# Optimization experiments

Measured on AMD Instinct MI355X. Metric: run time of the kernel, lower is better.

Reference implementation:

```python
import jax, jax.numpy as jnp
import numpy as np

N_NODES = 50000
N_EDGES = 800000
D_IN, D_HID, D_OUT = 128, 64, 64


def gcn_conv(x, W, b, src, dst, num_nodes):
    """PyG-style GCNConv: add self-loops, symmetric norm, aggregate at target.
    src/dst already include self-loops. x: [N, Din], W: [Din, Dout]."""
    xw = x @ W  # transform first (Din -> Dout), like PyG
    ew = jnp.ones(src.shape[0], dtype=x.dtype)
    deg = jax.ops.segment_sum(ew, dst, num_segments=num_nodes)
    dis = jnp.where(deg > 0, jax.lax.rsqrt(deg), 0.0)  # deg^{-1/2}
    norm = dis[src] * ew * dis[dst]  # [E+N]
    msgs = norm[:, None] * xw[src]  # gather source features
    out = jax.ops.segment_sum(msgs, dst, num_segments=num_nodes)
    return out + b


def setup_inputs() -> dict:
    key = jax.random.key(0)
    ks = jax.random.split(key, 8)
    x = jax.random.normal(ks[0], (N_NODES, D_IN), dtype=jnp.float32)
    edge_index = jax.random.randint(ks[1], (2, N_EDGES), 0, N_NODES, dtype=jnp.int64)
    W1 = jax.random.normal(ks[2], (D_IN, D_HID), dtype=jnp.float32) * (1.0 / np.sqrt(D_IN))
    b1 = jnp.zeros((D_HID,), dtype=jnp.float32)
    W2 = jax.random.normal(ks[3], (D_HID, D_HID), dtype=jnp.float32) * (1.0 / np.sqrt(D_HID))
    b2 = jnp.zeros((D_HID,), dtype=jnp.float32)
    W3 = jax.random.normal(ks[4], (D_HID, D_OUT), dtype=jnp.float32) * (1.0 / np.sqrt(D_HID))
    b3 = jnp.zeros((D_OUT,), dtype=jnp.float32)
    return {"x": x, "edge_index": edge_index, "W1": W1, "b1": b1,
            "W2": W2, "b2": b2, "W3": W3, "b3": b3}


def reference(x, edge_index, W1, b1, W2, b2, W3, b3):
    # Add self-loops once (shared by all layers), as PyG GCNConv does per layer.
    loop = jnp.arange(N_NODES, dtype=edge_index.dtype)
    src = jnp.concatenate([edge_index[0], loop])
    dst = jnp.concatenate([edge_index[1], loop])
    # Layer 1 + ReLU (dropout is identity in eval mode)
    h = gcn_conv(x, W1, b1, src, dst, N_NODES)
    h = jax.nn.relu(h)
    # Layer 2 + ReLU
    h = gcn_conv(h, W2, b2, src, dst, N_NODES)
    h = jax.nn.relu(h)
    # Layer 3 (no activation)
    out = gcn_conv(h, W3, b3, src, dst, N_NODES)
    return out
```

## Files before the change

kernel.cpp:

```cpp
#include <hip/hip_runtime.h>
#include <hip/hip_fp16.h>

#define N_NODES 50000
#define N_PAD   50048
#define N_EDGES 800000
#define D_IN    128
#define D_HID   64

#define NB         196
#define EB_CHUNK   4096
#define BIN_BLOCKS 196
#define ESTRIDE    4864
#define CSTRIDE    (ESTRIDE + 256)

typedef __bf16 bf16x8 __attribute__((ext_vector_type(8)));
typedef float  f32x4  __attribute__((ext_vector_type(4)));


template <int K>
__device__ __forceinline__ void pack_w(const float* __restrict__ W,
                                       __bf16* __restrict__ Bh, __bf16* __restrict__ Bl, int i) {
  constexpr int KS = K / 32;
  int j = i & 7, lane = (i >> 3) & 63, rest = i >> 9;
  int ct = rest / KS, ks = rest - ct * KS;
  int k = ks * 32 + ((lane >> 4) << 3) + j;
  int c = ct * 16 + (lane & 15);
  float v = W[k * 64 + c];
  __bf16 hb = (__bf16)v;
  Bh[i] = hb;
  Bl[i] = (__bf16)(v - (float)hb);
}


__global__ __launch_bounds__(256) void k_bins_sw(const int* __restrict__ src,
                                                 const int* __restrict__ dst,
                                                 unsigned* __restrict__ bucket_fill,
                                                 unsigned* __restrict__ temp,
                                                 const float* __restrict__ W1,
                                                 const float* __restrict__ W2,
                                                 const float* __restrict__ W3,
                                                 __bf16* __restrict__ Wh1, __bf16* __restrict__ Wl1,
                                                 __bf16* __restrict__ Wh2, __bf16* __restrict__ Wl2,
                                                 __bf16* __restrict__ Wh3, __bf16* __restrict__ Wl3) {
  __shared__ unsigned lh[256], lcur[256];
  int blk = blockIdx.x, t = threadIdx.x;
  if (blk >= BIN_BLOCKS) {
    int b = blk - BIN_BLOCKS;
    if (b < 32)      pack_w<D_IN >(W1, Wh1, Wl1, b * 256 + t);
    else if (b < 48) pack_w<D_HID>(W2, Wh2, Wl2, (b - 32) * 256 + t);
    else             pack_w<D_HID>(W3, Wh3, Wl3, (b - 48) * 256 + t);
    return;
  }
  lh[t] = 0;
  __syncthreads();
  int base = blk * EB_CHUNK;
  int endv = min(base + EB_CHUNK, N_EDGES);
  for (int e = base + t; e < endv; e += 256)
    atomicAdd(&lh[((unsigned)dst[e]) >> 8], 1u);
  __syncthreads();
  unsigned c = lh[t];
  lcur[t] = t * ESTRIDE + (c ? atomicAdd(&bucket_fill[t], c) : 0u);
  __syncthreads();
  for (int e = base + t; e < endv; e += 256) {
    unsigned d = (unsigned)dst[e];
    unsigned pos = atomicAdd(&lcur[d >> 8], 1u);
    temp[pos] = (unsigned)src[e] | ((d & 255u) << 16);
  }
}


template <int K, bool FIRST>
__device__ __forceinline__ void gemm_body(int bid,
                                          const float* __restrict__ Xf,
                                          const __bf16* __restrict__ Bh,
                                          const __bf16* __restrict__ Bl,
                                          __half* __restrict__ Y) {
  constexpr int KS = K / 32;
  const int tid  = threadIdx.x;
  const int wave = tid >> 6;
  const int lane = tid & 63;
  const int row0 = bid * 64 + wave * 16;
  const int row_a = min(row0 + (lane & 15), N_NODES - 1);
  const int q8 = (lane >> 4) << 3;

  f32x4 acc[4];
#pragma unroll
  for (int ct = 0; ct < 4; ct++) acc[ct] = (f32x4){0.f, 0.f, 0.f, 0.f};

#pragma unroll
  for (int ks = 0; ks < KS; ks++) {
    bf16x8 ah, al;
    const float4* xr4 = reinterpret_cast<const float4*>(Xf + (size_t)row_a * K);
    float4 f0 = xr4[ks * 8 + (q8 >> 2) + 0];
    float4 f1 = xr4[ks * 8 + (q8 >> 2) + 1];
#pragma unroll
    for (int j = 0; j < 4; j++) {
      float a0 = (&f0.x)[j], a1 = (&f1.x)[j];
      __bf16 h0 = (__bf16)a0, h1 = (__bf16)a1;
      ah[j] = h0;     al[j] = (__bf16)(a0 - (float)h0);
      ah[4 + j] = h1; al[4 + j] = (__bf16)(a1 - (float)h1);
    }
#pragma unroll
    for (int ct = 0; ct < 4; ct++) {
      bf16x8 bh = *reinterpret_cast<const bf16x8*>(Bh + (size_t)((ct * KS + ks) * 64 + lane) * 8);
      bf16x8 bl = *reinterpret_cast<const bf16x8*>(Bl + (size_t)((ct * KS + ks) * 64 + lane) * 8);
      acc[ct] = __builtin_amdgcn_mfma_f32_16x16x32_bf16(ah, bh, acc[ct], 0, 0, 0);
      acc[ct] = __builtin_amdgcn_mfma_f32_16x16x32_bf16(ah, bl, acc[ct], 0, 0, 0);
      acc[ct] = __builtin_amdgcn_mfma_f32_16x16x32_bf16(al, bh, acc[ct], 0, 0, 0);
    }
  }

  const int rbase = row0 + ((lane >> 4) << 2);
  const int c     = lane & 15;
#pragma unroll
  for (int ct = 0; ct < 4; ct++)
#pragma unroll
    for (int r = 0; r < 4; r++) {
      int row = rbase + r;
      if (row < N_NODES)
        Y[(size_t)row * 64 + ct * 16 + c] = __float2half_rn(acc[ct][r]);
    }
}


__global__ __launch_bounds__(256) void k_csr_gemm1(const unsigned* __restrict__ temp,
                                                   const unsigned* __restrict__ bucket_fill,
                                                   unsigned* __restrict__ rowptr,
                                                   unsigned* __restrict__ rowend,
                                                   float* __restrict__ dis,
                                                   unsigned short* __restrict__ csr,
                                                   const float* __restrict__ x,
                                                   const __bf16* __restrict__ Wh1,
                                                   const __bf16* __restrict__ Wl1,
                                                   __half* __restrict__ xw) {
  __shared__ unsigned hist[256], sscan[256], lfill[256];
  if (blockIdx.x >= NB) {
    gemm_body<D_IN, true>(blockIdx.x - NB, x, Wh1, Wl1, xw);
    return;
  }
  int b = blockIdx.x, t = threadIdx.x;
  unsigned ebase = b * ESTRIDE, ecnt = bucket_fill[b], cbase = b * CSTRIDE;
  int nodes = min(256, N_NODES - b * 256);
  hist[t] = 0;
  __syncthreads();
  for (unsigned i = t; i < ecnt; i += 256)
    atomicAdd(&hist[(temp[ebase + i] >> 16) & 255u], 1u);
  __syncthreads();
  unsigned deg = (t < nodes) ? hist[t] + 1u : 0u;
  sscan[t] = deg;
  __syncthreads();
  for (int off = 1; off < 256; off <<= 1) {
    unsigned v = (t >= off) ? sscan[t - off] : 0u;
    __syncthreads();
    sscan[t] += v;
    __syncthreads();
  }
  unsigned excl = sscan[t] - deg;
  if (t < nodes) {
    int node = b * 256 + t;
    rowptr[node] = cbase + excl;
    rowend[node] = cbase + excl + deg;
    dis[node] = rsqrtf((float)deg);
    csr[cbase + excl] = (unsigned short)node;
  }
  lfill[t] = excl + 1u;
  __syncthreads();
  for (unsigned i = t; i < ecnt; i += 256) {
    unsigned v = temp[ebase + i];
    unsigned d = (v >> 16) & 255u;
    unsigned pos = atomicAdd(&lfill[d], 1u);
    csr[cbase + pos] = (unsigned short)(v & 0xFFFFu);
  }
}


__device__ __forceinline__ void agg_core(int node, int lane, int sub, int grp,
                                         const float4* __restrict__ XW4,
                                         const unsigned* __restrict__ rowptr,
                                         const unsigned* __restrict__ rowend,
                                         const unsigned short* __restrict__ csr,
                                         const float* __restrict__ dis,
                                         float* __restrict__ accout) {
  const float disd = dis[node];
  unsigned beg = rowptr[node], end = rowend[node];
  float acc0[8] = {0,0,0,0,0,0,0,0};
  float acc1[8] = {0,0,0,0,0,0,0,0};

  for (unsigned j = beg; j < end; j += 64) {
    int nj = (int)min(64u, end - j);
    unsigned s = 0u; float nrm = 0.f;
    if (lane < nj) {
      s = csr[j + lane];
      nrm = dis[s] * disd;
    }
    for (int k = 0; k < nj; k += 16) {
      int e0 = k + grp;
      unsigned s0 = (unsigned)__shfl((int)s, e0);
      float    n0 = __shfl(nrm, e0);
      float4 v0 = XW4[(size_t)s0 * 8 + sub];
      const __half2* h0 = reinterpret_cast<const __half2*>(&v0);
#pragma unroll
      for (int q = 0; q < 4; q++) {
        float2 f = __half22float2(h0[q]);
        acc0[2*q]   += n0 * f.x;
        acc0[2*q+1] += n0 * f.y;
      }
      if (k + 8 < nj) {
        int e1 = k + grp + 8;
        unsigned s1 = (unsigned)__shfl((int)s, e1);
        float    n1 = __shfl(nrm, e1);
        float4 v1 = XW4[(size_t)s1 * 8 + sub];
        const __half2* h1 = reinterpret_cast<const __half2*>(&v1);
#pragma unroll
        for (int q = 0; q < 4; q++) {
          float2 f = __half22float2(h1[q]);
          acc1[2*q]   += n1 * f.x;
          acc1[2*q+1] += n1 * f.y;
        }
      }
    }
  }

#pragma unroll
  for (int i = 0; i < 8; i++) {
    float a = acc0[i] + acc1[i];
    a += __shfl_xor(a, 8);
    a += __shfl_xor(a, 16);
    a += __shfl_xor(a, 32);
    accout[i] = a;
  }
}


__global__ __launch_bounds__(1024) void k_agg_gemm(const float4* __restrict__ XW4,
                                                   const unsigned* __restrict__ rowptr,
                                                   const unsigned* __restrict__ rowend,
                                                   const unsigned short* __restrict__ csr,
                                                   const float* __restrict__ dis,
                                                   const float4* __restrict__ bias4,
                                                   const __bf16* __restrict__ Bh,
                                                   const __bf16* __restrict__ Bl,
                                                   __half* __restrict__ Y) {
  __shared__ float hld[16][68];
  const int wave = threadIdx.x >> 6;
  const int lane = threadIdx.x & 63;
  const int sub  = lane & 7;
  const int grp  = lane >> 3;
  const int node = blockIdx.x * 16 + wave;

  float acc[8];
  agg_core(node, lane, sub, grp, XW4, rowptr, rowend, csr, dis, acc);

  if (grp == 0) {
    float4 ba = bias4[sub * 2], bb = bias4[sub * 2 + 1];
    acc[0] += ba.x; acc[1] += ba.y; acc[2] += ba.z; acc[3] += ba.w;
    acc[4] += bb.x; acc[5] += bb.y; acc[6] += bb.z; acc[7] += bb.w;
    float4 o0, o1;
    o0.x = fmaxf(acc[0], 0.f); o0.y = fmaxf(acc[1], 0.f);
    o0.z = fmaxf(acc[2], 0.f); o0.w = fmaxf(acc[3], 0.f);
    o1.x = fmaxf(acc[4], 0.f); o1.y = fmaxf(acc[5], 0.f);
    o1.z = fmaxf(acc[6], 0.f); o1.w = fmaxf(acc[7], 0.f);
    *reinterpret_cast<float4*>(&hld[wave][sub * 8])     = o0;
    *reinterpret_cast<float4*>(&hld[wave][sub * 8 + 4]) = o1;
  }
  __syncthreads();

  if (wave < 4) {
    const int ct = wave;
    const int r16 = lane & 15;
    const int q8  = (lane >> 4) << 3;
    f32x4 gacc = (f32x4){0.f, 0.f, 0.f, 0.f};
#pragma unroll
    for (int ks = 0; ks < 2; ks++) {
      float4 f0 = *reinterpret_cast<const float4*>(&hld[r16][ks * 32 + q8]);
      float4 f1 = *reinterpret_cast<const float4*>(&hld[r16][ks * 32 + q8 + 4]);
      bf16x8 ah, al;
#pragma unroll
      for (int j = 0; j < 4; j++) {
        float a0 = (&f0.x)[j], a1 = (&f1.x)[j];
        __bf16 h0 = (__bf16)a0, h1 = (__bf16)a1;
        ah[j] = h0;     al[j] = (__bf16)(a0 - (float)h0);
        ah[4 + j] = h1; al[4 + j] = (__bf16)(a1 - (float)h1);
      }
      bf16x8 bh = *reinterpret_cast<const bf16x8*>(Bh + (size_t)((ct * 2 + ks) * 64 + lane) * 8);
      bf16x8 bl = *reinterpret_cast<const bf16x8*>(Bl + (size_t)((ct * 2 + ks) * 64 + lane) * 8);
      gacc = __builtin_amdgcn_mfma_f32_16x16x32_bf16(ah, bh, gacc, 0, 0, 0);
      gacc = __builtin_amdgcn_mfma_f32_16x16x32_bf16(ah, bl, gacc, 0, 0, 0);
      gacc = __builtin_amdgcn_mfma_f32_16x16x32_bf16(al, bh, gacc, 0, 0, 0);
    }
    const int rbase = blockIdx.x * 16 + ((lane >> 4) << 2);
    const int c     = lane & 15;
#pragma unroll
    for (int r = 0; r < 4; r++)
      Y[(size_t)(rbase + r) * 64 + ct * 16 + c] = __float2half_rn(gacc[r]);
  }
}


__global__ __launch_bounds__(256) void k_agg3(const float4* __restrict__ XW4,
                                              const unsigned* __restrict__ rowptr,
                                              const unsigned* __restrict__ rowend,
                                              const unsigned short* __restrict__ csr,
                                              const float* __restrict__ dis,
                                              const float4* __restrict__ bias4,
                                              float4* __restrict__ OUT4) {
  int node = (int)((blockIdx.x * blockDim.x + threadIdx.x) >> 6);
  int lane = threadIdx.x & 63;
  if (node >= N_NODES) return;
  const int sub = lane & 7;
  const int grp = lane >> 3;

  float acc[8];
  agg_core(node, lane, sub, grp, XW4, rowptr, rowend, csr, dis, acc);

  if (grp == 0) {
    float4 ba = bias4[sub * 2], bb = bias4[sub * 2 + 1];
    float4 o0 = {acc[0] + ba.x, acc[1] + ba.y, acc[2] + ba.z, acc[3] + ba.w};
    float4 o1 = {acc[4] + bb.x, acc[5] + bb.y, acc[6] + bb.z, acc[7] + bb.w};
    OUT4[(size_t)node * 16 + sub * 2]     = o0;
    OUT4[(size_t)node * 16 + sub * 2 + 1] = o1;
  }
}


extern "C" void kernel_launch(void* const* d_in, const int* in_sizes, int n_in,
                              void* d_out, int out_size, void* d_ws, size_t ws_size,
                              hipStream_t stream) {
  const float* x    = (const float*)d_in[0];
  const int*   eidx = (const int*)d_in[1];
  const float* W1   = (const float*)d_in[2];
  const float* b1   = (const float*)d_in[3];
  const float* W2   = (const float*)d_in[4];
  const float* b2   = (const float*)d_in[5];
  const float* W3   = (const float*)d_in[6];
  const float* b3   = (const float*)d_in[7];
  float* out = (float*)d_out;

  const int* e_src = eidx;
  const int* e_dst = eidx + N_EDGES;

  size_t off = 0;
  auto alloc = [&](size_t bytes) -> void* {
    void* p = (char*)d_ws + off;
    off += (bytes + 255) & ~(size_t)255;
    return p;
  };
  unsigned*       rowptr = (unsigned*)alloc((size_t)N_NODES * 4);
  unsigned*       rowend = (unsigned*)alloc((size_t)N_NODES * 4);
  float*          dis    = (float*)alloc((size_t)N_NODES * 4);
  unsigned short* csr    = (unsigned short*)alloc((size_t)NB * CSTRIDE * 2);
  unsigned*       temp   = (unsigned*)alloc((size_t)NB * ESTRIDE * 4);
  unsigned*       bfill  = (unsigned*)alloc(256 * 4);
  __half*         xwA    = (__half*)alloc((size_t)N_PAD * 64 * 2);
  __half*         xwB    = (__half*)alloc((size_t)N_PAD * 64 * 2);
  __bf16*         Wh1    = (__bf16*)alloc((size_t)D_IN * 64 * 2);
  __bf16*         Wl1    = (__bf16*)alloc((size_t)D_IN * 64 * 2);
  __bf16*         Wh2    = (__bf16*)alloc((size_t)D_HID * 64 * 2);
  __bf16*         Wl2    = (__bf16*)alloc((size_t)D_HID * 64 * 2);
  __bf16*         Wh3    = (__bf16*)alloc((size_t)D_HID * 64 * 2);
  __bf16*         Wl3    = (__bf16*)alloc((size_t)D_HID * 64 * 2);

  const int gemm_grid  = N_PAD / 64;
  const int fused_grid = N_NODES / 16;
  const int agg_grid   = (N_NODES * 64 + 255) / 256;

  hipMemsetAsync(bfill, 0, 256 * 4, stream);
  k_bins_sw<<<BIN_BLOCKS + 64, 256, 0, stream>>>(e_src, e_dst, bfill, temp,
                                                 W1, W2, W3, Wh1, Wl1, Wh2, Wl2, Wh3, Wl3);
  k_csr_gemm1<<<NB + gemm_grid, 256, 0, stream>>>(temp, bfill, rowptr, rowend,
                                                  dis, csr, x, Wh1, Wl1, xwA);
  k_agg_gemm<<<fused_grid, 1024, 0, stream>>>((const float4*)xwA, rowptr, rowend, csr, dis,
                                              (const float4*)b1, Wh2, Wl2, xwB);
  k_agg_gemm<<<fused_grid, 1024, 0, stream>>>((const float4*)xwB, rowptr, rowend, csr, dis,
                                              (const float4*)b2, Wh3, Wl3, xwA);
  k_agg3<<<agg_grid, 256, 0, stream>>>((const float4*)xwA, rowptr, rowend, csr, dis,
                                       (const float4*)b3, (float4*)out);
}
```

Measured before the change: 125.3 us.

## Fuse all GCN stages into one cooperative persistent kernel with grid syncs

```diff
diff --git a/kernel.cpp b/kernel.cpp
--- a/kernel.cpp
+++ b/kernel.cpp
@@ -1,5 +1,8 @@
 #include <hip/hip_runtime.h>
 #include <hip/hip_fp16.h>
+#include <hip/hip_cooperative_groups.h>
+
+namespace cg = cooperative_groups;
 
 #define N_NODES 50000
 #define N_PAD   50048
@@ -9,12 +12,22 @@
 
 #define NB         196
 #define EB_CHUNK   4096
-#define BIN_BLOCKS 196
 #define ESTRIDE    4864
 #define CSTRIDE    (ESTRIDE + 256)
 
 typedef __bf16 bf16x8 __attribute__((ext_vector_type(8)));
 typedef float  f32x4  __attribute__((ext_vector_type(4)));
+
+struct MegaParams {
+  const int* e_src; const int* e_dst;
+  unsigned* bfill; unsigned* temp;
+  const float* W1; const float* W2; const float* W3;
+  __bf16 *Wh1, *Wl1, *Wh2, *Wl2, *Wh3, *Wl3;
+  unsigned* rowptr; unsigned* rowend; float* dis; unsigned short* csr;
+  const float* x; __half* xwA; __half* xwB;
+  const float4 *b1, *b2, *b3;
+  float4* out;
+};
 
 
 template <int K>
@@ -32,51 +45,12 @@
 }
 
 
-__global__ __launch_bounds__(256) void k_bins_sw(const int* __restrict__ src,
-                                                 const int* __restrict__ dst,
-                                                 unsigned* __restrict__ bucket_fill,
-                                                 unsigned* __restrict__ temp,
-                                                 const float* __restrict__ W1,
-                                                 const float* __restrict__ W2,
-                                                 const float* __restrict__ W3,
-                                                 __bf16* __restrict__ Wh1, __bf16* __restrict__ Wl1,
-                                                 __bf16* __restrict__ Wh2, __bf16* __restrict__ Wl2,
-                                                 __bf16* __restrict__ Wh3, __bf16* __restrict__ Wl3) {
-  __shared__ unsigned lh[256], lcur[256];
-  int blk = blockIdx.x, t = threadIdx.x;
-  if (blk >= BIN_BLOCKS) {
-    int b = blk - BIN_BLOCKS;
-    if (b < 32)      pack_w<D_IN >(W1, Wh1, Wl1, b * 256 + t);
-    else if (b < 48) pack_w<D_HID>(W2, Wh2, Wl2, (b - 32) * 256 + t);
-    else             pack_w<D_HID>(W3, Wh3, Wl3, (b - 48) * 256 + t);
-    return;
-  }
-  lh[t] = 0;
-  __syncthreads();
-  int base = blk * EB_CHUNK;
-  int endv = min(base + EB_CHUNK, N_EDGES);
-  for (int e = base + t; e < endv; e += 256)
-    atomicAdd(&lh[((unsigned)dst[e]) >> 8], 1u);
-  __syncthreads();
-  unsigned c = lh[t];
-  lcur[t] = t * ESTRIDE + (c ? atomicAdd(&bucket_fill[t], c) : 0u);
-  __syncthreads();
-  for (int e = base + t; e < endv; e += 256) {
-    unsigned d = (unsigned)dst[e];
-    unsigned pos = atomicAdd(&lcur[d >> 8], 1u);
-    temp[pos] = (unsigned)src[e] | ((d & 255u) << 16);
-  }
-}
-
-
-template <int K, bool FIRST>
-__device__ __forceinline__ void gemm_body(int bid,
+__device__ __forceinline__ void gemm1_sub(int bid, int tid,
                                           const float* __restrict__ Xf,
                                           const __bf16* __restrict__ Bh,
                                           const __bf16* __restrict__ Bl,
                                           __half* __restrict__ Y) {
-  constexpr int KS = K / 32;
-  const int tid  = threadIdx.x;
+  constexpr int K = D_IN, KS = K / 32;
   const int wave = tid >> 6;
   const int lane = tid & 63;
   const int row0 = bid * 64 + wave * 16;
@@ -120,57 +94,6 @@
       if (row < N_NODES)
         Y[(size_t)row * 64 + ct * 16 + c] = __float2half_rn(acc[ct][r]);
     }
-}
-
-
-__global__ __launch_bounds__(256) void k_csr_gemm1(const unsigned* __restrict__ temp,
-                                                   const unsigned* __restrict__ bucket_fill,
-                                                   unsigned* __restrict__ rowptr,
-                                                   unsigned* __restrict__ rowend,
-                                                   float* __restrict__ dis,
-                                                   unsigned short* __restrict__ csr,
-                                                   const float* __restrict__ x,
-                                                   const __bf16* __restrict__ Wh1,
-                                                   const __bf16* __restrict__ Wl1,
-                                                   __half* __restrict__ xw) {
-  __shared__ unsigned hist[256], sscan[256], lfill[256];
-  if (blockIdx.x >= NB) {
-    gemm_body<D_IN, true>(blockIdx.x - NB, x, Wh1, Wl1, xw);
-    return;
-  }
-  int b = blockIdx.x, t = threadIdx.x;
-  unsigned ebase = b * ESTRIDE, ecnt = bucket_fill[b], cbase = b * CSTRIDE;
-  int nodes = min(256, N_NODES - b * 256);
-  hist[t] = 0;
-  __syncthreads();
-  for (unsigned i = t; i < ecnt; i += 256)
-    atomicAdd(&hist[(temp[ebase + i] >> 16) & 255u], 1u);
-  __syncthreads();
-  unsigned deg = (t < nodes) ? hist[t] + 1u : 0u;
-  sscan[t] = deg;
-  __syncthreads();
-  for (int off = 1; off < 256; off <<= 1) {
-    unsigned v = (t >= off) ? sscan[t - off] : 0u;
-    __syncthreads();
-    sscan[t] += v;
-    __syncthreads();
-  }
-  unsigned excl = sscan[t] - deg;
-  if (t < nodes) {
-    int node = b * 256 + t;
-    rowptr[node] = cbase + excl;
-    rowend[node] = cbase + excl + deg;
-    dis[node] = rsqrtf((float)deg);
-    csr[cbase + excl] = (unsigned short)node;
-  }
-  lfill[t] = excl + 1u;
-  __syncthreads();
-  for (unsigned i = t; i < ecnt; i += 256) {
-    unsigned v = temp[ebase + i];
-    unsigned d = (v >> 16) & 255u;
-    unsigned pos = atomicAdd(&lfill[d], 1u);
-    csr[cbase + pos] = (unsigned short)(v & 0xFFFFu);
-  }
 }
 
 
@@ -232,21 +155,21 @@
 }
 
 
-__global__ __launch_bounds__(1024) void k_agg_gemm(const float4* __restrict__ XW4,
-                                                   const unsigned* __restrict__ rowptr,
-                                                   const unsigned* __restrict__ rowend,
-                                                   const unsigned short* __restrict__ csr,
-                                                   const float* __restrict__ dis,
-                                                   const float4* __restrict__ bias4,
-                                                   const __bf16* __restrict__ Bh,
-                                                   const __bf16* __restrict__ Bl,
-                                                   __half* __restrict__ Y) {
-  __shared__ float hld[16][68];
-  const int wave = threadIdx.x >> 6;
-  const int lane = threadIdx.x & 63;
+__device__ __forceinline__ void agg_gemm_tile(int v, int t, float (*hld)[68],
+                                              const float4* __restrict__ XW4,
+                                              const unsigned* __restrict__ rowptr,
+                                              const unsigned* __restrict__ rowend,
+                                              const unsigned short* __restrict__ csr,
+                                              const float* __restrict__ dis,
+                                              const float4* __restrict__ bias4,
+                                              const __bf16* __restrict__ Bh,
+                                              const __bf16* __restrict__ Bl,
+                                              __half* __restrict__ Y) {
+  const int wave = t >> 6;
+  const int lane = t & 63;
   const int sub  = lane & 7;
   const int grp  = lane >> 3;
-  const int node = blockIdx.x * 16 + wave;
+  const int node = v * 16 + wave;
 
   float acc[8];
   agg_core(node, lane, sub, grp, XW4, rowptr, rowend, csr, dis, acc);
@@ -288,37 +211,120 @@
       gacc = __builtin_amdgcn_mfma_f32_16x16x32_bf16(ah, bl, gacc, 0, 0, 0);
       gacc = __builtin_amdgcn_mfma_f32_16x16x32_bf16(al, bh, gacc, 0, 0, 0);
     }
-    const int rbase = blockIdx.x * 16 + ((lane >> 4) << 2);
+    const int rbase = v * 16 + ((lane >> 4) << 2);
     const int c     = lane & 15;
 #pragma unroll
     for (int r = 0; r < 4; r++)
       Y[(size_t)(rbase + r) * 64 + ct * 16 + c] = __float2half_rn(gacc[r]);
   }
-}
-
-
-__global__ __launch_bounds__(256) void k_agg3(const float4* __restrict__ XW4,
-                                              const unsigned* __restrict__ rowptr,
-                                              const unsigned* __restrict__ rowend,
-                                              const unsigned short* __restrict__ csr,
-                                              const float* __restrict__ dis,
-                                              const float4* __restrict__ bias4,
-                                              float4* __restrict__ OUT4) {
-  int node = (int)((blockIdx.x * blockDim.x + threadIdx.x) >> 6);
-  int lane = threadIdx.x & 63;
-  if (node >= N_NODES) return;
-  const int sub = lane & 7;
-  const int grp = lane >> 3;
-
-  float acc[8];
-  agg_core(node, lane, sub, grp, XW4, rowptr, rowend, csr, dis, acc);
-
-  if (grp == 0) {
-    float4 ba = bias4[sub * 2], bb = bias4[sub * 2 + 1];
-    float4 o0 = {acc[0] + ba.x, acc[1] + ba.y, acc[2] + ba.z, acc[3] + ba.w};
-    float4 o1 = {acc[4] + bb.x, acc[5] + bb.y, acc[6] + bb.z, acc[7] + bb.w};
-    OUT4[(size_t)node * 16 + sub * 2]     = o0;
-    OUT4[(size_t)node * 16 + sub * 2 + 1] = o1;
+  __syncthreads();
+}
+
+
+__global__ __launch_bounds__(1024) void k_mega(MegaParams p) {
+  cg::grid_group grid = cg::this_grid();
+  __shared__ unsigned smem[4 * 768];
+  __shared__ float hld[16][68];
+  const int bid = blockIdx.x;
+  const int t   = threadIdx.x;
+  const int sb  = t >> 8, st = t & 255;
+
+  if (bid == 0 && t < 256) p.bfill[t] = 0;
+  grid.sync();
+
+  if (bid < 49) {
+    int v = bid * 4 + sb;
+    unsigned* lh   = smem + sb * 512;
+    unsigned* lcur = lh + 256;
+    lh[st] = 0;
+    __syncthreads();
+    int base = v * EB_CHUNK;
+    int endv = min(base + EB_CHUNK, N_EDGES);
+    for (int e = base + st; e < endv; e += 256)
+      atomicAdd(&lh[((unsigned)p.e_dst[e]) >> 8], 1u);
+    __syncthreads();
+    unsigned c = lh[st];
+    lcur[st] = st * ESTRIDE + (c ? atomicAdd(&p.bfill[st], c) : 0u);
+    __syncthreads();
+    for (int e = base + st; e < endv; e += 256) {
+      unsigned d = (unsigned)p.e_dst[e];
+      unsigned pos = atomicAdd(&lcur[d >> 8], 1u);
+      p.temp[pos] = (unsigned)p.e_src[e] | ((d & 255u) << 16);
+    }
+  } else if (bid < 65) {
+    int b = (bid - 49) * 4 + sb;
+    if (b < 32)      pack_w<D_IN >(p.W1, p.Wh1, p.Wl1, b * 256 + st);
+    else if (b < 48) pack_w<D_HID>(p.W2, p.Wh2, p.Wl2, (b - 32) * 256 + st);
+    else             pack_w<D_HID>(p.W3, p.Wh3, p.Wl3, (b - 48) * 256 + st);
+  }
+  grid.sync();
+
+  if (bid < 49) {
+    int b = bid * 4 + sb;
+    unsigned* hist  = smem + sb * 768;
+    unsigned* sscan = hist + 256;
+    unsigned* lfill = sscan + 256;
+    unsigned ebase = b * ESTRIDE, ecnt = p.bfill[b], cbase = b * CSTRIDE;
+    int nodes = min(256, N_NODES - b * 256);
+    hist[st] = 0;
+    __syncthreads();
+    for (unsigned i = st; i < ecnt; i += 256)
+      atomicAdd(&hist[(p.temp[ebase + i] >> 16) & 255u], 1u);
+    __syncthreads();
+    unsigned deg = (st < nodes) ? hist[st] + 1u : 0u;
+    sscan[st] = deg;
+    __syncthreads();
+    for (int off = 1; off < 256; off <<= 1) {
+      unsigned v2 = (st >= off) ? sscan[st - off] : 0u;
+      __syncthreads();
+      sscan[st] += v2;
+      __syncthreads();
+    }
+    unsigned excl = sscan[st] - deg;
+    if (st < nodes) {
+      int node = b * 256 + st;
+      p.rowptr[node] = cbase + excl;
+      p.rowend[node] = cbase + excl + deg;
+      p.dis[node] = rsqrtf((float)deg);
+      p.csr[cbase + excl] = (unsigned short)node;
+    }
+    lfill[st] = excl + 1u;
+    __syncthreads();
+    for (unsigned i = st; i < ecnt; i += 256) {
+      unsigned v2 = p.temp[ebase + i];
+      unsigned d = (v2 >> 16) & 255u;
+      unsigned pos = atomicAdd(&lfill[d], 1u);
+      p.csr[cbase + pos] = (unsigned short)(v2 & 0xFFFFu);
+    }
+  } else {
+    int v = (bid - 49) * 4 + sb;
+    if (v < 782) gemm1_sub(v, st, p.x, p.Wh1, p.Wl1, p.xwA);
+  }
+  grid.sync();
+
+  for (int v = bid; v < 3125; v += 256)
+    agg_gemm_tile(v, t, hld, (const float4*)p.xwA, p.rowptr, p.rowend, p.csr, p.dis,
+                  p.b1, p.Wh2, p.Wl2, p.xwB);
+  grid.sync();
+
+  for (int v = bid; v < 3125; v += 256)
+    agg_gemm_tile(v, t, hld, (const float4*)p.xwB, p.rowptr, p.rowend, p.csr, p.dis,
+                  p.b2, p.Wh3, p.Wl3, p.xwA);
+  grid.sync();
+
+  for (int v = bid; v < 3125; v += 256) {
+    const int wave = t >> 6, lane = t & 63;
+    const int sub = lane & 7, grp = lane >> 3;
+    const int node = v * 16 + wave;
+    float acc[8];
+    agg_core(node, lane, sub, grp, (const float4*)p.xwA, p.rowptr, p.rowend, p.csr, p.dis, acc);
+    if (grp == 0) {
+      float4 ba = p.b3[sub * 2], bb = p.b3[sub * 2 + 1];
+      float4 o0 = {acc[0] + ba.x, acc[1] + ba.y, acc[2] + ba.z, acc[3] + ba.w};
+      float4 o1 = {acc[4] + bb.x, acc[5] + bb.y, acc[6] + bb.z, acc[7] + bb.w};
+      p.out[(size_t)node * 16 + sub * 2]     = o0;
+      p.out[(size_t)node * 16 + sub * 2 + 1] = o1;
+    }
   }
 }
 
@@ -334,10 +340,6 @@
   const float* b2   = (const float*)d_in[5];
   const float* W3   = (const float*)d_in[6];
   const float* b3   = (const float*)d_in[7];
-  float* out = (float*)d_out;
-
-  const int* e_src = eidx;
-  const int* e_dst = eidx + N_EDGES;
 
   size_t off = 0;
   auto alloc = [&](size_t bytes) -> void* {
@@ -360,19 +362,16 @@
   __bf16*         Wh3    = (__bf16*)alloc((size_t)D_HID * 64 * 2);
   __bf16*         Wl3    = (__bf16*)alloc((size_t)D_HID * 64 * 2);
 
-  const int gemm_grid  = N_PAD / 64;
-  const int fused_grid = N_NODES / 16;
-  const int agg_grid   = (N_NODES * 64 + 255) / 256;
-
-  hipMemsetAsync(bfill, 0, 256 * 4, stream);
-  k_bins_sw<<<BIN_BLOCKS + 64, 256, 0, stream>>>(e_src, e_dst, bfill, temp,
-                                                 W1, W2, W3, Wh1, Wl1, Wh2, Wl2, Wh3, Wl3);
-  k_csr_gemm1<<<NB + gemm_grid, 256, 0, stream>>>(temp, bfill, rowptr, rowend,
-                                                  dis, csr, x, Wh1, Wl1, xwA);
-  k_agg_gemm<<<fused_grid, 1024, 0, stream>>>((const float4*)xwA, rowptr, rowend, csr, dis,
-                                              (const float4*)b1, Wh2, Wl2, xwB);
-  k_agg_gemm<<<fused_grid, 1024, 0, stream>>>((const float4*)xwB, rowptr, rowend, csr, dis,
-                                              (const float4*)b2, Wh3, Wl3, xwA);
-  k_agg3<<<agg_grid, 256, 0, stream>>>((const float4*)xwA, rowptr, rowend, csr, dis,
-                                       (const float4*)b3, (float4*)out);
-}
+  MegaParams mp;
+  mp.e_src = eidx; mp.e_dst = eidx + N_EDGES;
+  mp.bfill = bfill; mp.temp = temp;
+  mp.W1 = W1; mp.W2 = W2; mp.W3 = W3;
+  mp.Wh1 = Wh1; mp.Wl1 = Wl1; mp.Wh2 = Wh2; mp.Wl2 = Wl2; mp.Wh3 = Wh3; mp.Wl3 = Wl3;
+  mp.rowptr = rowptr; mp.rowend = rowend; mp.dis = dis; mp.csr = csr;
+  mp.x = x; mp.xwA = xwA; mp.xwB = xwB;
+  mp.b1 = (const float4*)b1; mp.b2 = (const float4*)b2; mp.b3 = (const float4*)b3;
+  mp.out = (float4*)d_out;
+
+  void* args[] = { &mp };
+  hipLaunchCooperativeKernel((const void*)k_mega, dim3(256), dim3(1024), args, 0, stream);
+}
```

Measured after the change: 307.2 us. 2.45x slower.
